# Kernel tuning notes

Measured on AMD Instinct MI355X. Metric: run time of the kernel, lower is better.

## Reference

```python
import jax, jax.numpy as jnp
import numpy as np

B, N, C, H = 4, 2048, 1024, 16
HD = C // H            # head dim = 64
HALF = HD // 2         # complex pairs per head = 32
VR = 32.0              # virtual_resolution
THETA = 10.0           # rope_theta


def _init_freqs():
    # mirrors init_3d_freqs_unified + per-axis replication with small noise
    rng = np.random.default_rng(0)
    idx = np.arange(HALF, dtype=np.float32)
    base = 1.0 / THETA ** (2.0 * idx / HD)                 # [HALF]
    angles = rng.uniform(0, 2 * np.pi, size=(H, 1)).astype(np.float32)
    per_head = base[None, :] * np.cos(angles)              # [H, HALF]
    freqs = np.repeat(per_head[None], 3, axis=0)           # [3, H, HALF]
    freqs = freqs + rng.normal(0, 0.01, freqs.shape).astype(np.float32)
    return jnp.asarray(freqs.reshape(3, H * HALF), dtype=jnp.float32)


def setup_inputs() -> dict:
    key = jax.random.key(0)
    ks = jax.random.split(key, 7)
    x = jax.random.normal(ks[0], (B, N, C), dtype=jnp.float32)
    t_x = jax.random.uniform(ks[1], (N,), dtype=jnp.float32)
    t_y = jax.random.uniform(ks[2], (N,), dtype=jnp.float32)
    t_z = jax.random.uniform(ks[3], (N,), dtype=jnp.float32)
    w_qkv = jax.random.normal(ks[4], (3 * C, C), dtype=jnp.float32) * (C ** -0.5)
    w_proj = jax.random.normal(ks[5], (C, C), dtype=jnp.float32) * (C ** -0.5)
    b_proj = jnp.zeros((C,), dtype=jnp.float32)
    freqs = _init_freqs()
    return {"x": x, "t_x": t_x, "t_y": t_y, "t_z": t_z,
            "w_qkv": w_qkv, "w_proj": w_proj, "b_proj": b_proj, "freqs": freqs}


def _normalize(t):
    # normalize_point_coords_3d with 'virtual_resolution'
    return (t - t.min()) / (t.max() - t.min() + 1e-8) * VR


def reference(x, t_x, t_y, t_z, w_qkv, w_proj, b_proj, freqs):
    # QKV projection (no bias)
    qkv = (x @ w_qkv.T).reshape(B, N, 3, H, HD).transpose(2, 0, 3, 1, 4)  # [3,B,H,N,HD]
    q, k, v = qkv[0], qkv[1], qkv[2]

    # mixed 3D RoPE angles: outer(t_axis, freqs[axis]) summed over axes
    tx, ty, tz = _normalize(t_x), _normalize(t_y), _normalize(t_z)
    ang = (tx[:, None] * freqs[0] + ty[:, None] * freqs[1] + tz[:, None] * freqs[2])  # [N, H*HALF]
    ang = ang.reshape(N, H, HALF).transpose(1, 0, 2)       # [H, N, HALF]
    cos, sin = jnp.cos(ang), jnp.sin(ang)

    def rotate(t):
        # complex multiply (a+ib)*(cos+isin) on even/odd pairs of last dim
        tr = t.reshape(B, H, N, HALF, 2)
        a, b = tr[..., 0], tr[..., 1]
        ra = a * cos - b * sin
        rb = a * sin + b * cos
        return jnp.stack([ra, rb], axis=-1).reshape(B, H, N, HD)

    q = rotate(q)
    k = rotate(k)

    scale = HD ** -0.5
    attn = jax.nn.softmax(jnp.einsum('bhnd,bhmd->bhnm', q * scale, k), axis=-1)
    out = jnp.einsum('bhnm,bhmd->bhnd', attn, v).transpose(0, 2, 1, 3).reshape(B, N, C)
    return out @ w_proj.T + b_proj
```

## Files before the change

### kernel.cpp

```cpp
#include <hip/hip_runtime.h>
#include <math.h>

#define BB 4
#define NN 2048
#define CC 1024
#define HH 16
#define HD 64
#define HALF 32
#define MM (BB*NN)
#define K3 (3*CC)
#define NF (HH*HALF)
#define NT (NN/64)

typedef __attribute__((ext_vector_type(8))) short bf16x8;
typedef __attribute__((ext_vector_type(4))) float f32x4;
typedef __attribute__((ext_vector_type(16))) float f32x16;
typedef __attribute__((ext_vector_type(4))) unsigned short u16x4;
typedef __attribute__((ext_vector_type(8))) unsigned short u16x8;
typedef __attribute__((ext_vector_type(4))) unsigned int u32x4;

#if __has_builtin(__builtin_amdgcn_exp2f)
#define EXP2(x) __builtin_amdgcn_exp2f(x)
#else
#define EXP2(x) exp2f(x)
#endif
#define AS1 __attribute__((address_space(1)))
#define AS3 __attribute__((address_space(3)))

__device__ __forceinline__ unsigned short f2bf(float f) {
    unsigned int u = __float_as_uint(f);
    unsigned int r = (u + 0x7FFFu + ((u >> 16) & 1u)) >> 16;
    return (unsigned short)r;
}

__global__ __launch_bounds__(256) void tnorm_kernel(const float* t_x, const float* t_y,
                                                    const float* t_z, float* tnorm) {
    int a = blockIdx.x;
    const float* t = (a == 0) ? t_x : ((a == 1) ? t_y : t_z);
    __shared__ float smn[256], smx[256];
    float mn = 1e30f, mx = -1e30f;
    for (int i = threadIdx.x; i < NN; i += 256) {
        float v = t[i];
        mn = fminf(mn, v);
        mx = fmaxf(mx, v);
    }
    smn[threadIdx.x] = mn; smx[threadIdx.x] = mx;
    __syncthreads();
    for (int s = 128; s > 0; s >>= 1) {
        if (threadIdx.x < s) {
            smn[threadIdx.x] = fminf(smn[threadIdx.x], smn[threadIdx.x + s]);
            smx[threadIdx.x] = fmaxf(smx[threadIdx.x], smx[threadIdx.x + s]);
        }
        __syncthreads();
    }
    float lo = smn[0];
    float sc = 32.0f / (smx[0] - lo + 1e-8f);
    for (int i = threadIdx.x; i < NN; i += 256)
        tnorm[a * NN + i] = (t[i] - lo) * sc;
}

__global__ __launch_bounds__(512) void angle_kernel(const float* freqs, const float* tnorm,
                                                    float* csT) {
    int n = blockIdx.x;
    int hf = threadIdx.x;
    float ang = tnorm[n] * freqs[hf]
              + tnorm[NN + n] * freqs[NF + hf]
              + tnorm[2 * NN + n] * freqs[2 * NF + hf];
    float2 cs;
    cs.x = cosf(ang);
    cs.y = sinf(ang);
    *(float2*)(csT + 2 * ((size_t)n * NF + hf)) = cs;
}

#define XBLK (MM * CC / 2048)
#define WQBLK (K3 * CC / 2048)
#define WPBLK (CC * CC / 2048)
__global__ __launch_bounds__(256) void cvt_all_kernel(const float* __restrict__ x,
                                                      const float* __restrict__ wq,
                                                      const float* __restrict__ wp,
                                                      unsigned short* __restrict__ xb,
                                                      unsigned short* __restrict__ wqb,
                                                      unsigned short* __restrict__ wpb) {
    int bid = blockIdx.x;
    const float* src;
    unsigned short* dst;
    if (bid < XBLK) { src = x; dst = xb; }
    else if (bid < XBLK + WQBLK) { src = wq; dst = wqb; bid -= XBLK; }
    else { src = wp; dst = wpb; bid -= XBLK + WQBLK; }
    int i = (bid * 256 + threadIdx.x) * 8;
    float4 a = *(const float4*)(src + i);
    float4 b = *(const float4*)(src + i + 4);
    u16x8 o;
    o[0] = f2bf(a.x); o[1] = f2bf(a.y); o[2] = f2bf(a.z); o[3] = f2bf(a.w);
    o[4] = f2bf(b.x); o[5] = f2bf(b.y); o[6] = f2bf(b.z); o[7] = f2bf(b.w);
    *(u16x8*)(dst + i) = o;
}

__global__ __launch_bounds__(256) void qkv_gemm_kernel(const unsigned short* __restrict__ A,
                                                       const unsigned short* __restrict__ Bw,
                                                       const float* __restrict__ csT,
                                                       unsigned short* __restrict__ qb,
                                                       unsigned short* __restrict__ kb,
                                                       unsigned short* __restrict__ vbT) {
    __shared__ unsigned short Asl[2][128 * 64];
    __shared__ unsigned short Bsl[2][128 * 64];
    const int tid = threadIdx.x;
    const int wv = tid >> 6, l = tid & 63;
    const int wm = wv >> 1, wn = wv & 1;
    const int lg = l >> 4, l15 = l & 15;
    const int m0 = blockIdx.x * 128, n0 = blockIdx.y * 128;

    const unsigned short* asrc[4];
    const unsigned short* bsrc[4];
#pragma unroll
    for (int i = 0; i < 4; i++) {
        int c = (wv * 4 + i) * 64 + l;
        int r = c >> 3, kc = c & 7;
        int sc = (kc ^ (r & 7)) * 8;
        asrc[i] = A + (size_t)(m0 + r) * CC + sc;
        bsrc[i] = Bw + (size_t)(n0 + r) * CC + sc;
    }

#define QSTAGE(buf) do { \
    _Pragma("unroll") \
    for (int i = 0; i < 4; i++) { \
        __builtin_amdgcn_global_load_lds((AS1 void*)asrc[i], (AS3 void*)(&Asl[buf][(wv * 4 + i) * 512]), 16, 0, 0); \
        __builtin_amdgcn_global_load_lds((AS1 void*)bsrc[i], (AS3 void*)(&Bsl[buf][(wv * 4 + i) * 512]), 16, 0, 0); \
        asrc[i] += 64; bsrc[i] += 64; \
    } \
} while (0)

#define QCOMPUTE(buf) do { \
    _Pragma("unroll") \
    for (int kc = 0; kc < 2; kc++) { \
        bf16x8 af[4], bfr[4]; \
        _Pragma("unroll") \
        for (int mi = 0; mi < 4; mi++) { \
            int r = wm * 64 + mi * 16 + l15; \
            af[mi] = *(const bf16x8*)(&Asl[buf][r * 64 + (((kc * 4 + lg) ^ (r & 7)) * 8)]); \
        } \
        _Pragma("unroll") \
        for (int nj = 0; nj < 4; nj++) { \
            int r = wn * 64 + nj * 16 + l15; \
            bfr[nj] = *(const bf16x8*)(&Bsl[buf][r * 64 + (((kc * 4 + lg) ^ (r & 7)) * 8)]); \
        } \
        _Pragma("unroll") \
        for (int mi = 0; mi < 4; mi++) \
            _Pragma("unroll") \
            for (int nj = 0; nj < 4; nj++) \
                acc[mi][nj] = __builtin_amdgcn_mfma_f32_16x16x32_bf16(af[mi], bfr[nj], acc[mi][nj], 0, 0, 0); \
    } \
} while (0)

#define QSYNC_PRE() do { \
    asm volatile("s_waitcnt vmcnt(8)" ::: "memory"); \
    __builtin_amdgcn_sched_barrier(0); \
    __builtin_amdgcn_s_barrier(); \
    __builtin_amdgcn_sched_barrier(0); \
} while (0)

#define QSYNC_POST() do { \
    __builtin_amdgcn_sched_barrier(0); \
    __builtin_amdgcn_s_barrier(); \
} while (0)

    f32x4 acc[4][4];
#pragma unroll
    for (int i = 0; i < 4; i++)
#pragma unroll
        for (int j = 0; j < 4; j++) acc[i][j] = f32x4{0.f, 0.f, 0.f, 0.f};

    QSTAGE(0);
    for (int ktb = 0; ktb < 16; ktb += 2) {
        QSTAGE(1);
        QSYNC_PRE();
        QCOMPUTE(0);
        QSYNC_POST();
        QSTAGE(0);
        QSYNC_PRE();
        QCOMPUTE(1);
        QSYNC_POST();
    }

    const int b_ = m0 >> 11;
    const int nrow0 = (m0 & (NN - 1));
#pragma unroll
    for (int nj = 0; nj < 4; nj++) {
        int oc = n0 + wn * 64 + nj * 16 + l15;
        int s = oc >> 10;
        int rr = oc & 1023;
        int h = rr >> 6;
        int d = rr & 63;
        int f = d >> 1;
#pragma unroll
        for (int mi = 0; mi < 4; mi++) {
            f32x4 v = acc[mi][nj];
            if (s == 2) {
                u16x4 vv;
#pragma unroll
                for (int reg = 0; reg < 4; reg++) vv[reg] = f2bf(v[reg]);
                int nb = nrow0 + wm * 64 + mi * 16 + lg * 4;
                *(u16x4*)(vbT + ((size_t)((b_ * HH + h) * HD + d)) * NN + nb) = vv;
            } else {
#pragma unroll
                for (int reg = 0; reg < 4; reg++) {
                    int m = m0 + wm * 64 + mi * 16 + lg * 4 + reg;
                    int n = m & (NN - 1);
                    float val = v[reg];
                    float partner = __shfl_xor(val, 1);
                    size_t base = (((size_t)(b_ * HH + h)) * NN + n) * HD + d;
                    float2 cs2 = *(const float2*)(csT + 2 * ((size_t)n * NF + h * HALF + f));
                    float res = ((d & 1) == 0) ? (val * cs2.x - partner * cs2.y)
                                               : (val * cs2.x + partner * cs2.y);
                    if (s == 0) res *= 0.18033688011112043f;
                    (s == 0 ? qb : kb)[base] = f2bf(res);
                }
            }
        }
    }
#undef QSTAGE
#undef QCOMPUTE
#undef QSYNC_PRE
#undef QSYNC_POST
}

template<int BUF>
__device__ __forceinline__ void attn_iter(
    unsigned short* LB, bool do_stage, int wv, int l31,
    const unsigned short*& kn0, const unsigned short*& kn1,
    const unsigned short*& vn0, const unsigned short*& vn1,
    const int (&so)[4], const bf16x8 (&qfA)[4], const bf16x8 (&qfB)[4],
    const f32x16& Z, const bf16x8& ones,
    f32x16& OA0, f32x16& OA1, f32x16& OB0, f32x16& OB1,
    f32x16& SsA, f32x16& SsB) {
    if (do_stage) {
        const int nb = (BUF ^ 1) * 4096;
        __builtin_amdgcn_global_load_lds((AS1 void*)kn0, (AS3 void*)(&LB[nb + (wv * 2 + 0) * 512]), 16, 0, 0);
        __builtin_amdgcn_global_load_lds((AS1 void*)kn1, (AS3 void*)(&LB[nb + (wv * 2 + 1) * 512]), 16, 0, 0);
        __builtin_amdgcn_global_load_lds((AS1 void*)vn0, (AS3 void*)(&LB[8192 + nb + (wv * 2 + 0) * 512]), 16, 0, 0);
        __builtin_amdgcn_global_load_lds((AS1 void*)vn1, (AS3 void*)(&LB[8192 + nb + (wv * 2 + 1) * 512]), 16, 0, 0);
        kn0 += 4096; kn1 += 4096; vn0 += 64; vn1 += 64;
    }
    f32x16 sA0, sA1, sB0, sB1;
    __builtin_amdgcn_s_setprio(1);
    {
        bf16x8 a0 = *(const bf16x8*)(LB + BUF * 4096 + l31 * 64 + so[0]);
        bf16x8 a1 = *(const bf16x8*)(LB + BUF * 4096 + (32 + l31) * 64 + so[0]);
        sA0 = __builtin_amdgcn_mfma_f32_32x32x16_bf16(a0, qfA[0], Z, 0, 0, 0);
        sA1 = __builtin_amdgcn_mfma_f32_32x32x16_bf16(a1, qfA[0], Z, 0, 0, 0);
        sB0 = __builtin_amdgcn_mfma_f32_32x32x16_bf16(a0, qfB[0], Z, 0, 0, 0);
        sB1 = __builtin_amdgcn_mfma_f32_32x32x16_bf16(a1, qfB[0], Z, 0, 0, 0);
    }
#pragma unroll
    for (int dc = 1; dc < 4; dc++) {
        bf16x8 a0 = *(const bf16x8*)(LB + BUF * 4096 + l31 * 64 + so[dc]);
        bf16x8 a1 = *(const bf16x8*)(LB + BUF * 4096 + (32 + l31) * 64 + so[dc]);
        sA0 = __builtin_amdgcn_mfma_f32_32x32x16_bf16(a0, qfA[dc], sA0, 0, 0, 0);
        sA1 = __builtin_amdgcn_mfma_f32_32x32x16_bf16(a1, qfA[dc], sA1, 0, 0, 0);
        sB0 = __builtin_amdgcn_mfma_f32_32x32x16_bf16(a0, qfB[dc], sB0, 0, 0, 0);
        sB1 = __builtin_amdgcn_mfma_f32_32x32x16_bf16(a1, qfB[dc], sB1, 0, 0, 0);
    }
    __builtin_amdgcn_s_setprio(0);
#pragma unroll
    for (int r = 0; r < 16; r++) {
        sA0[r] = EXP2(sA0[r]); sA1[r] = EXP2(sA1[r]);
        sB0[r] = EXP2(sB0[r]); sB1[r] = EXP2(sB1[r]);
    }
#pragma unroll
    for (int r = 0; r < 8; r++) {
        unsigned u0, u1, u2, u3;
        asm("v_cvt_pk_bf16_f32 %0, %1, %2" : "=v"(u0) : "v"(sA0[2 * r]), "v"(sA0[2 * r + 1]));
        asm("v_cvt_pk_bf16_f32 %0, %1, %2" : "=v"(u1) : "v"(sA1[2 * r]), "v"(sA1[2 * r + 1]));
        asm("v_cvt_pk_bf16_f32 %0, %1, %2" : "=v"(u2) : "v"(sB0[2 * r]), "v"(sB0[2 * r + 1]));
        asm("v_cvt_pk_bf16_f32 %0, %1, %2" : "=v"(u3) : "v"(sB1[2 * r]), "v"(sB1[2 * r + 1]));
        sA0[2 * r] = __uint_as_float(u0);
        sA1[2 * r] = __uint_as_float(u1);
        sB0[2 * r] = __uint_as_float(u2);
        sB1[2 * r] = __uint_as_float(u3);
    }
    __builtin_amdgcn_s_setprio(1);
#pragma unroll
    for (int kc = 0; kc < 4; kc++) {
        const int bs = (kc & 1) * 8;
        bf16x8 pfA, pfB;
        {
            float e0 = (kc < 2) ? sA0[bs + 0] : sA1[bs + 0];
            float e4 = (kc < 2) ? sA0[bs + 4] : sA1[bs + 4];
            float e2 = (kc < 2) ? sA0[bs + 2] : sA1[bs + 2];
            float e6 = (kc < 2) ? sA0[bs + 6] : sA1[bs + 6];
            auto uA = __builtin_amdgcn_permlane32_swap(__float_as_uint(e0), __float_as_uint(e4), false, false);
            auto uB = __builtin_amdgcn_permlane32_swap(__float_as_uint(e2), __float_as_uint(e6), false, false);
            u32x4 t; t.x = uA[0]; t.y = uB[0]; t.z = uA[1]; t.w = uB[1];
            pfA = __builtin_bit_cast(bf16x8, t);
        }
        {
            float e0 = (kc < 2) ? sB0[bs + 0] : sB1[bs + 0];
            float e4 = (kc < 2) ? sB0[bs + 4] : sB1[bs + 4];
            float e2 = (kc < 2) ? sB0[bs + 2] : sB1[bs + 2];
            float e6 = (kc < 2) ? sB0[bs + 6] : sB1[bs + 6];
            auto uA = __builtin_amdgcn_permlane32_swap(__float_as_uint(e0), __float_as_uint(e4), false, false);
            auto uB = __builtin_amdgcn_permlane32_swap(__float_as_uint(e2), __float_as_uint(e6), false, false);
            u32x4 t; t.x = uA[0]; t.y = uB[0]; t.z = uA[1]; t.w = uB[1];
            pfB = __builtin_bit_cast(bf16x8, t);
        }
        bf16x8 va  = *(const bf16x8*)(LB + 8192 + BUF * 4096 + l31 * 64 + so[kc]);
        bf16x8 vb2 = *(const bf16x8*)(LB + 8192 + BUF * 4096 + (32 + l31) * 64 + so[kc]);
        OA0 = __builtin_amdgcn_mfma_f32_32x32x16_bf16(va,  pfA, OA0, 0, 0, 0);
        OA1 = __builtin_amdgcn_mfma_f32_32x32x16_bf16(vb2, pfA, OA1, 0, 0, 0);
        OB0 = __builtin_amdgcn_mfma_f32_32x32x16_bf16(va,  pfB, OB0, 0, 0, 0);
        OB1 = __builtin_amdgcn_mfma_f32_32x32x16_bf16(vb2, pfB, OB1, 0, 0, 0);
        SsA = __builtin_amdgcn_mfma_f32_32x32x16_bf16(ones, pfA, SsA, 0, 0, 0);
        SsB = __builtin_amdgcn_mfma_f32_32x32x16_bf16(ones, pfB, SsB, 0, 0, 0);
    }
    __builtin_amdgcn_s_setprio(0);
    __syncthreads();
}

__global__ __launch_bounds__(256, 2) void attn_mfma_kernel(const unsigned short* __restrict__ qbp,
                                                           const unsigned short* __restrict__ kbp,
                                                           const unsigned short* __restrict__ vtp,
                                                           unsigned short* __restrict__ aout) {
    __shared__ unsigned short LB[4 * 4096];
    const int tid = threadIdx.x;
    const int wv = tid >> 6;
    const int l = tid & 63;
    const int l31 = l & 31, hi = l >> 5;

    const int wg = blockIdx.x;
    const int Lidx = (wg & 7) * 64 + (wg >> 3);
    const int bh = Lidx >> 3;
    const int q0 = (Lidx & 7) * 256;

    const unsigned short* qp = qbp + (size_t)bh * (NN * HD);
    const unsigned short* kp = kbp + (size_t)bh * (NN * HD);
    const unsigned short* vp = vtp + (size_t)bh * (NN * HD);

    const int r0 = (wv * 2 + 0) * 8 + (l >> 3);
    const int r1 = (wv * 2 + 1) * 8 + (l >> 3);
    const int c0 = ((l & 7) ^ (r0 & 7)) * 8;
    const int c1 = ((l & 7) ^ (r1 & 7)) * 8;
    const unsigned short* kn0 = kp + r0 * HD + c0;
    const unsigned short* kn1 = kp + r1 * HD + c1;
    const unsigned short* vn0 = vp + (size_t)r0 * NN + c0;
    const unsigned short* vn1 = vp + (size_t)r1 * NN + c1;

    __builtin_amdgcn_global_load_lds((AS1 void*)kn0, (AS3 void*)(&LB[(wv * 2 + 0) * 512]), 16, 0, 0);
    __builtin_amdgcn_global_load_lds((AS1 void*)kn1, (AS3 void*)(&LB[(wv * 2 + 1) * 512]), 16, 0, 0);
    __builtin_amdgcn_global_load_lds((AS1 void*)vn0, (AS3 void*)(&LB[8192 + (wv * 2 + 0) * 512]), 16, 0, 0);
    __builtin_amdgcn_global_load_lds((AS1 void*)vn1, (AS3 void*)(&LB[8192 + (wv * 2 + 1) * 512]), 16, 0, 0);
    kn0 += 4096; kn1 += 4096; vn0 += 64; vn1 += 64;

    const unsigned short* qr = qp + (size_t)(q0 + wv * 64 + l31) * HD;
    bf16x8 qfA[4], qfB[4];
#pragma unroll
    for (int dc = 0; dc < 4; dc++) {
        qfA[dc] = *(const bf16x8*)(qr + dc * 16 + hi * 8);
        qfB[dc] = *(const bf16x8*)(qr + 32 * HD + dc * 16 + hi * 8);
    }

    int so[4];
#pragma unroll
    for (int i = 0; i < 4; i++) so[i] = ((2 * i + hi) ^ (l31 & 7)) * 8;

    f32x16 Z;
#pragma unroll
    for (int r = 0; r < 16; r++) Z[r] = 0.0f;
    f32x16 OA0 = Z, OA1 = Z, OB0 = Z, OB1 = Z, SsA = Z, SsB = Z;
    bf16x8 ones;
#pragma unroll
    for (int j = 0; j < 8; j++) ones[j] = (short)0x3F80;

    __syncthreads();

    for (int ktb = 0; ktb < NT; ktb += 2) {
        attn_iter<0>(LB, true, wv, l31, kn0, kn1, vn0, vn1, so, qfA, qfB,
                     Z, ones, OA0, OA1, OB0, OB1, SsA, SsB);
        attn_iter<1>(LB, ktb + 2 < NT, wv, l31, kn0, kn1, vn0, vn1, so, qfA, qfB,
                     Z, ones, OA0, OA1, OB0, OB1, SsA, SsB);
    }

    const int b_ = bh >> 4, hh = bh & 15;
    const float invA = 1.0f / SsA[0], invB = 1.0f / SsB[0];
    const size_t mrowA = (size_t)(b_ * NN + q0 + wv * 64 + l31) * CC + hh * HD;
    const size_t mrowB = mrowA + (size_t)32 * CC;
#pragma unroll
    for (int rq = 0; rq < 4; rq++) {
        u16x4 a0, a1, b0, b1;
#pragma unroll
        for (int j = 0; j < 4; j++) {
            a0[j] = f2bf(OA0[rq * 4 + j] * invA);
            a1[j] = f2bf(OA1[rq * 4 + j] * invA);
            b0[j] = f2bf(OB0[rq * 4 + j] * invB);
            b1[j] = f2bf(OB1[rq * 4 + j] * invB);
        }
        *(u16x4*)(aout + mrowA + rq * 8 + hi * 4) = a0;
        *(u16x4*)(aout + mrowA + 32 + rq * 8 + hi * 4) = a1;
        *(u16x4*)(aout + mrowB + rq * 8 + hi * 4) = b0;
        *(u16x4*)(aout + mrowB + 32 + rq * 8 + hi * 4) = b1;
    }
}

__global__ __launch_bounds__(256) void proj_gemm_kernel(const unsigned short* __restrict__ A,
                                                        const unsigned short* __restrict__ Bw,
                                                        const float* __restrict__ bp,
                                                        float* __restrict__ out) {
    __shared__ unsigned short Asl[128 * 64];
    __shared__ unsigned short Bsl[128 * 64];
    const int tid = threadIdx.x;
    const int wv = tid >> 6, l = tid & 63;
    const int wm = wv >> 1, wn = wv & 1;
    const int lg = l >> 4, l15 = l & 15;
    const int m0 = blockIdx.x * 128, n0 = blockIdx.y * 128;

    f32x4 acc[4][4];
#pragma unroll
    for (int i = 0; i < 4; i++)
#pragma unroll
        for (int j = 0; j < 4; j++) acc[i][j] = f32x4{0.f, 0.f, 0.f, 0.f};

    for (int kt = 0; kt < CC; kt += 64) {
        __syncthreads();
#pragma unroll
        for (int i = 0; i < 4; i++) {
            int c = (wv * 4 + i) * 64 + l;
            int r = c >> 3, kc = c & 7;
            int sc = kt + ((kc ^ (r & 7)) * 8);
            __builtin_amdgcn_global_load_lds(
                (AS1 void*)(A + (size_t)(m0 + r) * CC + sc),
                (AS3 void*)(&Asl[(wv * 4 + i) * 512]), 16, 0, 0);
            __builtin_amdgcn_global_load_lds(
                (AS1 void*)(Bw + (size_t)(n0 + r) * CC + sc),
                (AS3 void*)(&Bsl[(wv * 4 + i) * 512]), 16, 0, 0);
        }
        __syncthreads();
#pragma unroll
        for (int kc = 0; kc < 2; kc++) {
            bf16x8 af[4], bfr[4];
#pragma unroll
            for (int mi = 0; mi < 4; mi++) {
                int r = wm * 64 + mi * 16 + l15;
                af[mi] = *(const bf16x8*)(&Asl[r * 64 + (((kc * 4 + lg) ^ (r & 7)) * 8)]);
            }
#pragma unroll
            for (int nj = 0; nj < 4; nj++) {
                int r = wn * 64 + nj * 16 + l15;
                bfr[nj] = *(const bf16x8*)(&Bsl[r * 64 + (((kc * 4 + lg) ^ (r & 7)) * 8)]);
            }
#pragma unroll
            for (int mi = 0; mi < 4; mi++)
#pragma unroll
                for (int nj = 0; nj < 4; nj++)
                    acc[mi][nj] = __builtin_amdgcn_mfma_f32_16x16x32_bf16(af[mi], bfr[nj], acc[mi][nj], 0, 0, 0);
        }
    }
    float bias[4];
#pragma unroll
    for (int nj = 0; nj < 4; nj++) bias[nj] = bp[n0 + wn * 64 + nj * 16 + l15];
#pragma unroll
    for (int mi = 0; mi < 4; mi++)
#pragma unroll
        for (int nj = 0; nj < 4; nj++) {
            int oc = n0 + wn * 64 + nj * 16 + l15;
#pragma unroll
            for (int reg = 0; reg < 4; reg++) {
                int m = m0 + wm * 64 + mi * 16 + lg * 4 + reg;
                out[(size_t)m * CC + oc] = acc[mi][nj][reg] + bias[nj];
            }
        }
}

extern "C" void kernel_launch(void* const* d_in, const int* in_sizes, int n_in,
                              void* d_out, int out_size, void* d_ws, size_t ws_size,
                              hipStream_t stream) {
    const float* x      = (const float*)d_in[0];
    const float* t_x    = (const float*)d_in[1];
    const float* t_y    = (const float*)d_in[2];
    const float* t_z    = (const float*)d_in[3];
    const float* w_qkv  = (const float*)d_in[4];
    const float* w_proj = (const float*)d_in[5];
    const float* b_proj = (const float*)d_in[6];
    const float* freqs  = (const float*)d_in[7];
    float* out = (float*)d_out;

    unsigned short* xb     = (unsigned short*)d_ws;
    unsigned short* wqkvb  = xb + (size_t)MM * CC;
    unsigned short* wprojb = wqkvb + (size_t)K3 * CC;
    unsigned short* qbuf   = wprojb + (size_t)CC * CC;
    unsigned short* kbuf   = qbuf + (size_t)BB * HH * NN * HD;
    unsigned short* vbT    = kbuf + (size_t)BB * HH * NN * HD;
    unsigned short* attnb  = vbT + (size_t)BB * HH * NN * HD;
    float* csT   = (float*)(attnb + (size_t)MM * CC);
    float* tnorm = csT + (size_t)2 * NN * NF;

    tnorm_kernel<<<3, 256, 0, stream>>>(t_x, t_y, t_z, tnorm);
    angle_kernel<<<NN, 512, 0, stream>>>(freqs, tnorm, csT);
    cvt_all_kernel<<<XBLK + WQBLK + WPBLK, 256, 0, stream>>>(x, w_qkv, w_proj,
                                                             xb, wqkvb, wprojb);
    qkv_gemm_kernel<<<dim3(MM / 128, K3 / 128), 256, 0, stream>>>(xb, wqkvb, csT,
                                                                  qbuf, kbuf, vbT);
    attn_mfma_kernel<<<512, 256, 0, stream>>>(qbuf, kbuf, vbT, attnb);
    proj_gemm_kernel<<<dim3(MM / 128, CC / 128), 256, 0, stream>>>(attnb, wprojb, b_proj, out);
}
```

Baseline: 199.9 us.

## Double-buffer proj GEMM and restructure attention K/V prefetch waits

The projection GEMM moves from a single-buffered loop with two __syncthreads per K-step to the same double-buffered global_load_lds pipeline the QKV GEMM uses, with shared stage/compute macros. The attention inner iteration now always issues the next K/V tile prefetch, waits with an explicit vmcnt(4) plus barrier so only the older tile must have landed, and replaces __syncthreads with a raw s_barrier. This aims to overlap global loads with MFMA work in both kernels. The costs are double LDS in the proj GEMM and an unconditional prefetch in the last attention iteration that reads past the final K/V tile.

```diff
diff --git a/kernel.cpp b/kernel.cpp
--- a/kernel.cpp
+++ b/kernel.cpp
@@ -96,6 +96,49 @@
     *(u16x8*)(dst + i) = o;
 }
 
+#define GSTAGE(Abuf, Bbuf, buf) do { \
+    _Pragma("unroll") \
+    for (int i = 0; i < 4; i++) { \
+        __builtin_amdgcn_global_load_lds((AS1 void*)asrc[i], (AS3 void*)(&Abuf[buf][(wv * 4 + i) * 512]), 16, 0, 0); \
+        __builtin_amdgcn_global_load_lds((AS1 void*)bsrc[i], (AS3 void*)(&Bbuf[buf][(wv * 4 + i) * 512]), 16, 0, 0); \
+        asrc[i] += 64; bsrc[i] += 64; \
+    } \
+} while (0)
+
+#define GCOMPUTE(Abuf, Bbuf, buf) do { \
+    _Pragma("unroll") \
+    for (int kc = 0; kc < 2; kc++) { \
+        bf16x8 af[4], bfr[4]; \
+        _Pragma("unroll") \
+        for (int mi = 0; mi < 4; mi++) { \
+            int r = wm * 64 + mi * 16 + l15; \
+            af[mi] = *(const bf16x8*)(&Abuf[buf][r * 64 + (((kc * 4 + lg) ^ (r & 7)) * 8)]); \
+        } \
+        _Pragma("unroll") \
+        for (int nj = 0; nj < 4; nj++) { \
+            int r = wn * 64 + nj * 16 + l15; \
+            bfr[nj] = *(const bf16x8*)(&Bbuf[buf][r * 64 + (((kc * 4 + lg) ^ (r & 7)) * 8)]); \
+        } \
+        _Pragma("unroll") \
+        for (int mi = 0; mi < 4; mi++) \
+            _Pragma("unroll") \
+            for (int nj = 0; nj < 4; nj++) \
+                acc[mi][nj] = __builtin_amdgcn_mfma_f32_16x16x32_bf16(af[mi], bfr[nj], acc[mi][nj], 0, 0, 0); \
+    } \
+} while (0)
+
+#define GSYNC_PRE() do { \
+    asm volatile("s_waitcnt vmcnt(8)" ::: "memory"); \
+    __builtin_amdgcn_sched_barrier(0); \
+    __builtin_amdgcn_s_barrier(); \
+    __builtin_amdgcn_sched_barrier(0); \
+} while (0)
+
+#define GSYNC_POST() do { \
+    __builtin_amdgcn_sched_barrier(0); \
+    __builtin_amdgcn_s_barrier(); \
+} while (0)
+
 __global__ __launch_bounds__(256) void qkv_gemm_kernel(const unsigned short* __restrict__ A,
                                                        const unsigned short* __restrict__ Bw,
                                                        const float* __restrict__ csT,
@@ -121,65 +164,22 @@
         bsrc[i] = Bw + (size_t)(n0 + r) * CC + sc;
     }
 
-#define QSTAGE(buf) do { \
-    _Pragma("unroll") \
-    for (int i = 0; i < 4; i++) { \
-        __builtin_amdgcn_global_load_lds((AS1 void*)asrc[i], (AS3 void*)(&Asl[buf][(wv * 4 + i) * 512]), 16, 0, 0); \
-        __builtin_amdgcn_global_load_lds((AS1 void*)bsrc[i], (AS3 void*)(&Bsl[buf][(wv * 4 + i) * 512]), 16, 0, 0); \
-        asrc[i] += 64; bsrc[i] += 64; \
-    } \
-} while (0)
-
-#define QCOMPUTE(buf) do { \
-    _Pragma("unroll") \
-    for (int kc = 0; kc < 2; kc++) { \
-        bf16x8 af[4], bfr[4]; \
-        _Pragma("unroll") \
-        for (int mi = 0; mi < 4; mi++) { \
-            int r = wm * 64 + mi * 16 + l15; \
-            af[mi] = *(const bf16x8*)(&Asl[buf][r * 64 + (((kc * 4 + lg) ^ (r & 7)) * 8)]); \
-        } \
-        _Pragma("unroll") \
-        for (int nj = 0; nj < 4; nj++) { \
-            int r = wn * 64 + nj * 16 + l15; \
-            bfr[nj] = *(const bf16x8*)(&Bsl[buf][r * 64 + (((kc * 4 + lg) ^ (r & 7)) * 8)]); \
-        } \
-        _Pragma("unroll") \
-        for (int mi = 0; mi < 4; mi++) \
-            _Pragma("unroll") \
-            for (int nj = 0; nj < 4; nj++) \
-                acc[mi][nj] = __builtin_amdgcn_mfma_f32_16x16x32_bf16(af[mi], bfr[nj], acc[mi][nj], 0, 0, 0); \
-    } \
-} while (0)
-
-#define QSYNC_PRE() do { \
-    asm volatile("s_waitcnt vmcnt(8)" ::: "memory"); \
-    __builtin_amdgcn_sched_barrier(0); \
-    __builtin_amdgcn_s_barrier(); \
-    __builtin_amdgcn_sched_barrier(0); \
-} while (0)
-
-#define QSYNC_POST() do { \
-    __builtin_amdgcn_sched_barrier(0); \
-    __builtin_amdgcn_s_barrier(); \
-} while (0)
-
     f32x4 acc[4][4];
 #pragma unroll
     for (int i = 0; i < 4; i++)
 #pragma unroll
         for (int j = 0; j < 4; j++) acc[i][j] = f32x4{0.f, 0.f, 0.f, 0.f};
 
-    QSTAGE(0);
+    GSTAGE(Asl, Bsl, 0);
     for (int ktb = 0; ktb < 16; ktb += 2) {
-        QSTAGE(1);
-        QSYNC_PRE();
-        QCOMPUTE(0);
-        QSYNC_POST();
-        QSTAGE(0);
-        QSYNC_PRE();
-        QCOMPUTE(1);
-        QSYNC_POST();
+        GSTAGE(Asl, Bsl, 1);
+        GSYNC_PRE();
+        GCOMPUTE(Asl, Bsl, 0);
+        GSYNC_POST();
+        GSTAGE(Asl, Bsl, 0);
+        GSYNC_PRE();
+        GCOMPUTE(Asl, Bsl, 1);
+        GSYNC_POST();
     }
 
     const int b_ = m0 >> 11;
@@ -218,22 +218,18 @@
             }
         }
     }
-#undef QSTAGE
-#undef QCOMPUTE
-#undef QSYNC_PRE
-#undef QSYNC_POST
 }
 
 template<int BUF>
 __device__ __forceinline__ void attn_iter(
-    unsigned short* LB, bool do_stage, int wv, int l31,
+    unsigned short* LB, int wv, int l31,
     const unsigned short*& kn0, const unsigned short*& kn1,
     const unsigned short*& vn0, const unsigned short*& vn1,
     const int (&so)[4], const bf16x8 (&qfA)[4], const bf16x8 (&qfB)[4],
     const f32x16& Z, const bf16x8& ones,
     f32x16& OA0, f32x16& OA1, f32x16& OB0, f32x16& OB1,
     f32x16& SsA, f32x16& SsB) {
-    if (do_stage) {
+    {
         const int nb = (BUF ^ 1) * 4096;
         __builtin_amdgcn_global_load_lds((AS1 void*)kn0, (AS3 void*)(&LB[nb + (wv * 2 + 0) * 512]), 16, 0, 0);
         __builtin_amdgcn_global_load_lds((AS1 void*)kn1, (AS3 void*)(&LB[nb + (wv * 2 + 1) * 512]), 16, 0, 0);
@@ -241,6 +237,11 @@
         __builtin_amdgcn_global_load_lds((AS1 void*)vn1, (AS3 void*)(&LB[8192 + nb + (wv * 2 + 1) * 512]), 16, 0, 0);
         kn0 += 4096; kn1 += 4096; vn0 += 64; vn1 += 64;
     }
+    asm volatile("s_waitcnt vmcnt(4)" ::: "memory");
+    __builtin_amdgcn_sched_barrier(0);
+    __builtin_amdgcn_s_barrier();
+    __builtin_amdgcn_sched_barrier(0);
+
     f32x16 sA0, sA1, sB0, sB1;
     __builtin_amdgcn_s_setprio(1);
     {
@@ -313,7 +314,8 @@
         SsB = __builtin_amdgcn_mfma_f32_32x32x16_bf16(ones, pfB, SsB, 0, 0, 0);
     }
     __builtin_amdgcn_s_setprio(0);
-    __syncthreads();
+    __builtin_amdgcn_sched_barrier(0);
+    __builtin_amdgcn_s_barrier();
 }
 
 __global__ __launch_bounds__(256, 2) void attn_mfma_kernel(const unsigned short* __restrict__ qbp,
@@ -373,9 +375,9 @@
     __syncthreads();
 
     for (int ktb = 0; ktb < NT; ktb += 2) {
-        attn_iter<0>(LB, true, wv, l31, kn0, kn1, vn0, vn1, so, qfA, qfB,
+        attn_iter<0>(LB, wv, l31, kn0, kn1, vn0, vn1, so, qfA, qfB,
                      Z, ones, OA0, OA1, OB0, OB1, SsA, SsB);
-        attn_iter<1>(LB, ktb + 2 < NT, wv, l31, kn0, kn1, vn0, vn1, so, qfA, qfB,
+        attn_iter<1>(LB, wv, l31, kn0, kn1, vn0, vn1, so, qfA, qfB,
                      Z, ones, OA0, OA1, OB0, OB1, SsA, SsB);
     }
 
@@ -404,55 +406,43 @@
                                                         const unsigned short* __restrict__ Bw,
                                                         const float* __restrict__ bp,
                                                         float* __restrict__ out) {
-    __shared__ unsigned short Asl[128 * 64];
-    __shared__ unsigned short Bsl[128 * 64];
+    __shared__ unsigned short Asl[2][128 * 64];
+    __shared__ unsigned short Bsl[2][128 * 64];
     const int tid = threadIdx.x;
     const int wv = tid >> 6, l = tid & 63;
     const int wm = wv >> 1, wn = wv & 1;
     const int lg = l >> 4, l15 = l & 15;
     const int m0 = blockIdx.x * 128, n0 = blockIdx.y * 128;
 
+    const unsigned short* asrc[4];
+    const unsigned short* bsrc[4];
+#pragma unroll
+    for (int i = 0; i < 4; i++) {
+        int c = (wv * 4 + i) * 64 + l;
+        int r = c >> 3, kc = c & 7;
+        int sc = (kc ^ (r & 7)) * 8;
+        asrc[i] = A + (size_t)(m0 + r) * CC + sc;
+        bsrc[i] = Bw + (size_t)(n0 + r) * CC + sc;
+    }
+
     f32x4 acc[4][4];
 #pragma unroll
     for (int i = 0; i < 4; i++)
 #pragma unroll
         for (int j = 0; j < 4; j++) acc[i][j] = f32x4{0.f, 0.f, 0.f, 0.f};
 
-    for (int kt = 0; kt < CC; kt += 64) {
-        __syncthreads();
-#pragma unroll
-        for (int i = 0; i < 4; i++) {
-            int c = (wv * 4 + i) * 64 + l;
-            int r = c >> 3, kc = c & 7;
-            int sc = kt + ((kc ^ (r & 7)) * 8);
-            __builtin_amdgcn_global_load_lds(
-                (AS1 void*)(A + (size_t)(m0 + r) * CC + sc),
-                (AS3 void*)(&Asl[(wv * 4 + i) * 512]), 16, 0, 0);
-            __builtin_amdgcn_global_load_lds(
-                (AS1 void*)(Bw + (size_t)(n0 + r) * CC + sc),
-                (AS3 void*)(&Bsl[(wv * 4 + i) * 512]), 16, 0, 0);
-        }
-        __syncthreads();
-#pragma unroll
-        for (int kc = 0; kc < 2; kc++) {
-            bf16x8 af[4], bfr[4];
-#pragma unroll
-            for (int mi = 0; mi < 4; mi++) {
-                int r = wm * 64 + mi * 16 + l15;
-                af[mi] = *(const bf16x8*)(&Asl[r * 64 + (((kc * 4 + lg) ^ (r & 7)) * 8)]);
-            }
-#pragma unroll
-            for (int nj = 0; nj < 4; nj++) {
-                int r = wn * 64 + nj * 16 + l15;
-                bfr[nj] = *(const bf16x8*)(&Bsl[r * 64 + (((kc * 4 + lg) ^ (r & 7)) * 8)]);
-            }
-#pragma unroll
-            for (int mi = 0; mi < 4; mi++)
-#pragma unroll
-                for (int nj = 0; nj < 4; nj++)
-                    acc[mi][nj] = __builtin_amdgcn_mfma_f32_16x16x32_bf16(af[mi], bfr[nj], acc[mi][nj], 0, 0, 0);
-        }
-    }
+    GSTAGE(Asl, Bsl, 0);
+    for (int ktb = 0; ktb < 16; ktb += 2) {
+        GSTAGE(Asl, Bsl, 1);
+        GSYNC_PRE();
+        GCOMPUTE(Asl, Bsl, 0);
+        GSYNC_POST();
+        GSTAGE(Asl, Bsl, 0);
+        GSYNC_PRE();
+        GCOMPUTE(Asl, Bsl, 1);
+        GSYNC_POST();
+    }
+
     float bias[4];
 #pragma unroll
     for (int nj = 0; nj < 4; nj++) bias[nj] = bp[n0 + wn * 64 + nj * 16 + l15];
```

After: 198.4 us (median of 2 runs). Within noise of the previous version (-0.7%).
